# Kernel tuning notes

Measured on AMD Instinct MI355X. Metric: run time of the kernel, lower is better.

Reference implementation:

```python
import jax, jax.numpy as jnp
import numpy as np

N, M, D, DV = 16384, 16384, 8, 16
BLOCK = 2048  # row tile size; kernel block is [BLOCK, M], never materialize full [N, M]


def setup_inputs() -> dict:
    key = jax.random.key(0)
    k1, k2, k3, k4 = jax.random.split(key, 4)
    ls = jax.random.uniform(k1, (D,), dtype=jnp.float32)          # per-dim lengthscale weights (positive)
    x = jax.random.normal(k2, (N, D), dtype=jnp.float32)
    y = jax.random.normal(k3, (M, D), dtype=jnp.float32)
    b = jax.random.normal(k4, (M, DV), dtype=jnp.float32)
    return {"ls": ls, "x": x, "y": y, "b": b}


def reference(ls, x, y, b):
    # Matern nu=2.5 kernel-weighted reduction:
    #   d2_ij = sum_d ls_d * (x_id - y_jd)^2
    #   K_ij  = (1 + c1*sqrt(d2) + c2*d2) * exp(-c1*sqrt(d2))   (c1=sqrt(5), c2=sqrt(5/3), as in the torch module)
    #   out_i = sum_j K_ij * b_j   -- computed in row tiles (KeOps-style online reduction)
    c1 = jnp.sqrt(jnp.asarray(5.0, x.dtype))
    c2 = jnp.sqrt(jnp.asarray(5.0 / 3.0, x.dtype))

    def row_block(xi):  # xi: [BLOCK, D]
        diff = xi[:, None, :] - y[None, :, :]                 # [BLOCK, M, D]
        d2 = jnp.einsum('d,bmd->bm', ls, diff * diff)         # [BLOCK, M]
        r = jnp.sqrt(d2)
        k = (1.0 + c1 * r + c2 * d2) * jnp.exp(-c1 * r)       # [BLOCK, M]
        return k @ b                                          # [BLOCK, DV]

    xb = x.reshape(-1, BLOCK, x.shape[1])                     # [N/BLOCK, BLOCK, D]
    out = jax.lax.map(row_block, xb)                          # [N/BLOCK, BLOCK, DV]
    return out.reshape(-1, b.shape[1])                        # [N, DV]
```

## Files before the change

### kernel.cpp

```cpp
#include <hip/hip_runtime.h>
#include <stdint.h>

#define NN 16384
#define MM 16384
#define DD 8
#define DV 16
#define WAVES 4
#define MT 2
#define ROWS_WAVE (MT * 16)
#define ROWS_BLK (WAVES * ROWS_WAVE)
#define JSPLIT 16
#define JCHUNK (MM / JSPLIT)
#define J32 (JCHUNK / 32)

typedef short bf8 __attribute__((ext_vector_type(8)));
typedef float f32x4 __attribute__((ext_vector_type(4)));

__device__ __forceinline__ unsigned short f2bf(float f) {
    union { float f; uint32_t u; } c; c.f = f;
    uint32_t u = c.u + 0x7FFF + ((c.u >> 16) & 1);
    return (unsigned short)(u >> 16);
}
__device__ __forceinline__ float bf2f(unsigned short h) {
    union { float f; uint32_t u; } c; c.u = ((uint32_t)h) << 16;
    return c.f;
}

__global__ __launch_bounds__(64) void prep_frags(const float* __restrict__ ls,
                                                 const float* __restrict__ y,
                                                 const float* __restrict__ b,
                                                 bf8* __restrict__ ytbl,
                                                 bf8* __restrict__ btbl,
                                                 float* __restrict__ sy) {
    const int tile = blockIdx.x;
    const int lane = threadIdx.x;
    const int n = lane & 15, quad = lane >> 4;

    float lsv[DD];
#pragma unroll
    for (int d = 0; d < DD; ++d) lsv[d] = ls[d];

    const float* yr = y + (size_t)(tile * 16 + n) * DD;
    float syv = 0.f;
    bf8 fr;
#pragma unroll
    for (int d = 0; d < DD; ++d) {
        float yv = yr[d];
        syv = fmaf(lsv[d] * yv, yv, syv);
        unsigned short yh = f2bf(yv);
        unsigned short yl = f2bf(yv - bf2f(yh));
        fr[d] = (short)(quad == 3 ? 0 : (quad == 2 ? yl : yh));
    }
    ytbl[tile * 64 + lane] = fr;
    if (quad == 0) sy[tile * 16 + n] = syv;

    if (tile < MM / 32) {
        bf8 bfr;
#pragma unroll
        for (int s = 0; s < 8; ++s) {
            float bv = b[(size_t)(tile * 32 + quad * 8 + s) * DV + n];
            bfr[s] = (short)f2bf(bv);
        }
        btbl[tile * 64 + lane] = bfr;
    }
}

__global__ __launch_bounds__(256, 8) void matern_mfma(const float* __restrict__ ls,
                                                      const float* __restrict__ x,
                                                      const bf8* __restrict__ ytbl,
                                                      const bf8* __restrict__ btbl,
                                                      const float* __restrict__ sy,
                                                      float* __restrict__ out) {
    const int t = threadIdx.x;
    const int lane = t & 63, wave = t >> 6;
    const int n = lane & 15, quad = lane >> 4;
    const int waverow = blockIdx.x * ROWS_BLK + wave * ROWS_WAVE;

    __shared__ __attribute__((aligned(16))) unsigned short klds[WAVES][MT][16][40];

    float lsv[DD];
#pragma unroll
    for (int d = 0; d < DD; ++d) lsv[d] = ls[d];

    bf8 afrag[MT];
#pragma unroll
    for (int mt = 0; mt < MT; ++mt) {
        const float* xr = x + (size_t)(waverow + mt * 16 + n) * DD;
#pragma unroll
        for (int d = 0; d < DD; ++d) {
            float xls = lsv[d] * xr[d];
            unsigned short xh = f2bf(xls);
            unsigned short xl = f2bf(xls - bf2f(xh));
            afrag[mt][d] = (short)(quad == 3 ? 0 : (quad == 1 ? xl : xh));
        }
    }

    float sxq[MT][4];
#pragma unroll
    for (int mt = 0; mt < MT; ++mt)
#pragma unroll
        for (int s = 0; s < 4; ++s) {
            const float* xr = x + (size_t)(waverow + mt * 16 + quad * 4 + s) * DD;
            float acc = 0.f;
#pragma unroll
            for (int d = 0; d < DD; ++d) acc = fmaf(lsv[d] * xr[d], xr[d], acc);
            sxq[mt][s] = acc;
        }

    const float c1 = 2.23606797749979f;
    const float c2 = 1.2909944487358056f;
    const float c3 = -3.2259641843312987f;

    f32x4 acc[MT];
#pragma unroll
    for (int mt = 0; mt < MT; ++mt) acc[mt] = (f32x4){0.f, 0.f, 0.f, 0.f};

    const int tile16base = blockIdx.y * (JCHUNK / 16);
    const int tile32base = blockIdx.y * (JCHUNK / 32);

#pragma unroll 1
    for (int it = 0; it < J32; ++it) {
        const int tl0 = tile16base + it * 2;
        bf8 yA = ytbl[(size_t)tl0 * 64 + lane];
        bf8 yB = ytbl[(size_t)(tl0 + 1) * 64 + lane];
        bf8 bb = btbl[(size_t)(tile32base + it) * 64 + lane];
        float syA = sy[tl0 * 16 + n];
        float syB = sy[(tl0 + 1) * 16 + n];

#pragma unroll
        for (int mt = 0; mt < MT; ++mt) {
            f32x4 z = (f32x4){0.f, 0.f, 0.f, 0.f};
            f32x4 s0 = __builtin_amdgcn_mfma_f32_16x16x32_bf16(afrag[mt], yA, z, 0, 0, 0);
            f32x4 s1 = __builtin_amdgcn_mfma_f32_16x16x32_bf16(afrag[mt], yB, z, 0, 0, 0);
#pragma unroll
            for (int s = 0; s < 4; ++s) {
                {
                    float d2 = fmaf(-2.f, s0[s], sxq[mt][s] + syA);
                    d2 = fmaxf(d2, 0.f);
                    float r = __builtin_amdgcn_sqrtf(d2);
                    float e = __builtin_amdgcn_exp2f(c3 * r);
                    float k = fmaf(c2, d2, fmaf(c1, r, 1.f)) * e;
                    klds[wave][mt][quad * 4 + s][n] = f2bf(k);
                }
                {
                    float d2 = fmaf(-2.f, s1[s], sxq[mt][s] + syB);
                    d2 = fmaxf(d2, 0.f);
                    float r = __builtin_amdgcn_sqrtf(d2);
                    float e = __builtin_amdgcn_exp2f(c3 * r);
                    float k = fmaf(c2, d2, fmaf(c1, r, 1.f)) * e;
                    klds[wave][mt][quad * 4 + s][n + 16] = f2bf(k);
                }
            }
        }
#pragma unroll
        for (int mt = 0; mt < MT; ++mt) {
            const bf8* kp = (const bf8*)&klds[wave][mt][n][quad * 8];
            acc[mt] = __builtin_amdgcn_mfma_f32_16x16x32_bf16(*kp, bb, acc[mt], 0, 0, 0);
        }
    }

#pragma unroll
    for (int mt = 0; mt < MT; ++mt)
#pragma unroll
        for (int s = 0; s < 4; ++s) {
            const int row = waverow + mt * 16 + quad * 4 + s;
            atomicAdd(out + (size_t)row * DV + n, acc[mt][s]);
        }
}

extern "C" void kernel_launch(void* const* d_in, const int* in_sizes, int n_in,
                              void* d_out, int out_size, void* d_ws, size_t ws_size,
                              hipStream_t stream) {
    const float* ls = (const float*)d_in[0];
    const float* x  = (const float*)d_in[1];
    const float* y  = (const float*)d_in[2];
    const float* b  = (const float*)d_in[3];
    float* out = (float*)d_out;

    char* ws = (char*)d_ws;
    bf8*   ytbl = (bf8*)ws;
    bf8*   btbl = (bf8*)(ws + (1 << 20));
    float* sy   = (float*)(ws + (1 << 20) + (512 << 10));

    hipMemsetAsync(d_out, 0, (size_t)out_size * sizeof(float), stream);
    prep_frags<<<MM / 16, 64, 0, stream>>>(ls, y, b, ytbl, btbl, sy);
    matern_mfma<<<dim3(NN / ROWS_BLK, JSPLIT), 256, 0, stream>>>(ls, x, ytbl, btbl, sy, out);
}
```

Baseline: 162.4 us.

## Fold squared norms into MFMA K-padding and use packed bf16 conversion

The x and y squared norms are moved into the unused fourth quad of the 32-wide bf16 fragments, scaled to -2 on the y side, so the MFMA produces the full squared distance directly. This removes the per-iteration sy loads and the per-element norm add/fma in the inner loop, and drops the sy workspace buffer. The k-to-bf16 conversion also uses a packed hardware convert when available. The cost is extra bf16 rounding of the norms, which are split into hi/lo parts, and of the -2*y terms, which may lower distance accuracy for large norms.

Result: faster. 151.7 us (-6.6%).

```diff
diff --git a/kernel.cpp b/kernel.cpp
--- a/kernel.cpp
+++ b/kernel.cpp
@@ -26,12 +26,13 @@
     return c.f;
 }
 
+#define BF16_ONE ((short)0x3F80)
+
 __global__ __launch_bounds__(64) void prep_frags(const float* __restrict__ ls,
                                                  const float* __restrict__ y,
                                                  const float* __restrict__ b,
                                                  bf8* __restrict__ ytbl,
-                                                 bf8* __restrict__ btbl,
-                                                 float* __restrict__ sy) {
+                                                 bf8* __restrict__ btbl) {
     const int tile = blockIdx.x;
     const int lane = threadIdx.x;
     const int n = lane & 15, quad = lane >> 4;
@@ -42,17 +43,32 @@
 
     const float* yr = y + (size_t)(tile * 16 + n) * DD;
     float syv = 0.f;
-    bf8 fr;
+    unsigned short yh[DD], yl[DD];
 #pragma unroll
     for (int d = 0; d < DD; ++d) {
         float yv = yr[d];
         syv = fmaf(lsv[d] * yv, yv, syv);
-        unsigned short yh = f2bf(yv);
-        unsigned short yl = f2bf(yv - bf2f(yh));
-        fr[d] = (short)(quad == 3 ? 0 : (quad == 2 ? yl : yh));
+        yh[d] = f2bf(yv);
+        yl[d] = f2bf(yv - bf2f(yh[d]));
+    }
+
+    bf8 fr;
+    if (quad < 3) {
+#pragma unroll
+        for (int d = 0; d < DD; ++d) {
+            unsigned short base = (quad == 2) ? yl[d] : yh[d];
+            fr[d] = (short)f2bf(-2.f * bf2f(base));
+        }
+    } else {
+        unsigned short sh = f2bf(syv);
+        unsigned short sl = f2bf(syv - bf2f(sh));
+        fr[0] = (short)sh;
+        fr[1] = (short)sl;
+        fr[2] = BF16_ONE;
+        fr[3] = BF16_ONE;
+        fr[4] = 0; fr[5] = 0; fr[6] = 0; fr[7] = 0;
     }
     ytbl[tile * 64 + lane] = fr;
-    if (quad == 0) sy[tile * 16 + n] = syv;
 
     if (tile < MM / 32) {
         bf8 bfr;
@@ -69,7 +85,6 @@
                                                       const float* __restrict__ x,
                                                       const bf8* __restrict__ ytbl,
                                                       const bf8* __restrict__ btbl,
-                                                      const float* __restrict__ sy,
                                                       float* __restrict__ out) {
     const int t = threadIdx.x;
     const int lane = t & 63, wave = t >> 6;
@@ -86,26 +101,32 @@
 #pragma unroll
     for (int mt = 0; mt < MT; ++mt) {
         const float* xr = x + (size_t)(waverow + mt * 16 + n) * DD;
+        float sx = 0.f;
+        unsigned short xh[DD], xl[DD];
 #pragma unroll
         for (int d = 0; d < DD; ++d) {
-            float xls = lsv[d] * xr[d];
-            unsigned short xh = f2bf(xls);
-            unsigned short xl = f2bf(xls - bf2f(xh));
-            afrag[mt][d] = (short)(quad == 3 ? 0 : (quad == 1 ? xl : xh));
-        }
-    }
-
-    float sxq[MT][4];
-#pragma unroll
-    for (int mt = 0; mt < MT; ++mt)
-#pragma unroll
-        for (int s = 0; s < 4; ++s) {
-            const float* xr = x + (size_t)(waverow + mt * 16 + quad * 4 + s) * DD;
-            float acc = 0.f;
-#pragma unroll
-            for (int d = 0; d < DD; ++d) acc = fmaf(lsv[d] * xr[d], xr[d], acc);
-            sxq[mt][s] = acc;
-        }
+            float xv = xr[d];
+            float xlsv = lsv[d] * xv;
+            sx = fmaf(xlsv, xv, sx);
+            xh[d] = f2bf(xlsv);
+            xl[d] = f2bf(xlsv - bf2f(xh[d]));
+        }
+        bf8 fr;
+        if (quad == 3) {
+            unsigned short sh = f2bf(sx);
+            unsigned short sl = f2bf(sx - bf2f(sh));
+            fr[0] = BF16_ONE;
+            fr[1] = BF16_ONE;
+            fr[2] = (short)sh;
+            fr[3] = (short)sl;
+            fr[4] = 0; fr[5] = 0; fr[6] = 0; fr[7] = 0;
+        } else {
+#pragma unroll
+            for (int d = 0; d < DD; ++d)
+                fr[d] = (short)((quad == 1) ? xl[d] : xh[d]);
+        }
+        afrag[mt] = fr;
+    }
 
     const float c1 = 2.23606797749979f;
     const float c2 = 1.2909944487358056f;
@@ -124,8 +145,6 @@
         bf8 yA = ytbl[(size_t)tl0 * 64 + lane];
         bf8 yB = ytbl[(size_t)(tl0 + 1) * 64 + lane];
         bf8 bb = btbl[(size_t)(tile32base + it) * 64 + lane];
-        float syA = sy[tl0 * 16 + n];
-        float syB = sy[(tl0 + 1) * 16 + n];
 
 #pragma unroll
         for (int mt = 0; mt < MT; ++mt) {
@@ -134,22 +153,26 @@
             f32x4 s1 = __builtin_amdgcn_mfma_f32_16x16x32_bf16(afrag[mt], yB, z, 0, 0, 0);
 #pragma unroll
             for (int s = 0; s < 4; ++s) {
-                {
-                    float d2 = fmaf(-2.f, s0[s], sxq[mt][s] + syA);
-                    d2 = fmaxf(d2, 0.f);
-                    float r = __builtin_amdgcn_sqrtf(d2);
-                    float e = __builtin_amdgcn_exp2f(c3 * r);
-                    float k = fmaf(c2, d2, fmaf(c1, r, 1.f)) * e;
-                    klds[wave][mt][quad * 4 + s][n] = f2bf(k);
-                }
-                {
-                    float d2 = fmaf(-2.f, s1[s], sxq[mt][s] + syB);
-                    d2 = fmaxf(d2, 0.f);
-                    float r = __builtin_amdgcn_sqrtf(d2);
-                    float e = __builtin_amdgcn_exp2f(c3 * r);
-                    float k = fmaf(c2, d2, fmaf(c1, r, 1.f)) * e;
-                    klds[wave][mt][quad * 4 + s][n + 16] = f2bf(k);
-                }
+                float d20 = fmaxf(s0[s], 0.f);
+                float d21 = fmaxf(s1[s], 0.f);
+                float r0 = __builtin_amdgcn_sqrtf(d20);
+                float r1 = __builtin_amdgcn_sqrtf(d21);
+                float e0 = __builtin_amdgcn_exp2f(c3 * r0);
+                float e1 = __builtin_amdgcn_exp2f(c3 * r1);
+                float k0 = fmaf(c2, d20, fmaf(c1, r0, 1.f)) * e0;
+                float k1 = fmaf(c2, d21, fmaf(c1, r1, 1.f)) * e1;
+#if __has_builtin(__builtin_amdgcn_cvt_pk_bf16_f32)
+                typedef __bf16 bf2v __attribute__((ext_vector_type(2)));
+                bf2v pk = __builtin_amdgcn_cvt_pk_bf16_f32(k0, k1);
+                union { bf2v v; unsigned short u[2]; } cv; cv.v = pk;
+                klds[wave][mt][quad * 4 + s][n] = cv.u[0];
+                klds[wave][mt][quad * 4 + s][n + 16] = cv.u[1];
+#else
+                klds[wave][mt][quad * 4 + s][n] =
+                    (unsigned short)((__float_as_uint(k0) + 0x8000u) >> 16);
+                klds[wave][mt][quad * 4 + s][n + 16] =
+                    (unsigned short)((__float_as_uint(k1) + 0x8000u) >> 16);
+#endif
             }
         }
 #pragma unroll
@@ -178,11 +201,10 @@
     float* out = (float*)d_out;
 
     char* ws = (char*)d_ws;
-    bf8*   ytbl = (bf8*)ws;
-    bf8*   btbl = (bf8*)(ws + (1 << 20));
-    float* sy   = (float*)(ws + (1 << 20) + (512 << 10));
+    bf8* ytbl = (bf8*)ws;
+    bf8* btbl = (bf8*)(ws + (1 << 20));
 
     hipMemsetAsync(d_out, 0, (size_t)out_size * sizeof(float), stream);
-    prep_frags<<<MM / 16, 64, 0, stream>>>(ls, y, b, ytbl, btbl, sy);
-    matern_mfma<<<dim3(NN / ROWS_BLK, JSPLIT), 256, 0, stream>>>(ls, x, ytbl, btbl, sy, out);
-}
+    prep_frags<<<MM / 16, 64, 0, stream>>>(ls, y, b, ytbl, btbl);
+    matern_mfma<<<dim3(NN / ROWS_BLK, JSPLIT), 256, 0, stream>>>(ls, x, ytbl, btbl, out);
+}
```
